# Kernel optimization log

Measured on AMD Instinct MI355X. Metric: run time of the kernel, lower is better.

The kernel has to match this reference:

```python
import jax, jax.numpy as jnp
import numpy as np

H, D, K, V, M = 32, 4096, 128, 128, 8191


def setup_inputs() -> dict:
    key = jax.random.key(0)
    ks = jax.random.split(key, 7)
    return {
        "x": jax.random.normal(ks[0], (D,), jnp.float32),
        "prev_K": jax.random.normal(ks[1], (H, M, K), jnp.float32),
        "prev_V": jax.random.normal(ks[2], (H, M, V), jnp.float32),
        "Wq": jax.random.normal(ks[3], (H, D, K), jnp.float32),
        "Wk": jax.random.normal(ks[4], (H, D, K), jnp.float32),
        "Wv": jax.random.normal(ks[5], (H, D, V), jnp.float32),
        "Wo": jax.random.normal(ks[6], (H, V, D), jnp.float32),
    }


def reference(x, prev_K, prev_V, Wq, Wk, Wv, Wo):
    # Single-token QKV projection
    q = jnp.einsum('d,hdk->hk', x, Wq)              # [h,k]
    k_new = jnp.einsum('d,hdk->hk', x, Wk)[:, None]  # [h,1,k]
    v_new = jnp.einsum('d,hdv->hv', x, Wv)[:, None]  # [h,1,v]
    # KV-cache append
    Kc = jnp.concatenate([prev_K, k_new], axis=1)    # [h,m+1,k]
    Vc = jnp.concatenate([prev_V, v_new], axis=1)    # [h,m+1,v]
    # Attention (no 1/sqrt(k) scaling, matching the original)
    logits = jnp.einsum('hk,hmk->hm', q, Kc)         # [h,m+1]
    weights = jax.nn.softmax(logits, axis=-1)
    o = jnp.einsum('hm,hmv->hv', weights, Vc)        # [h,v]
    # Output projection
    y = jnp.einsum('hv,hvd->d', o, Wo)               # [d]
    return (y, Kc, Vc)
```

## Files before the change

kernel.cpp:

```cpp
#include <hip/hip_runtime.h>
#include <hip/hip_bf16.h>
#include <math.h>

#define H_  32
#define D_  4096
#define K_  128
#define V_  128
#define M_  8191
#define MC_ 8192

typedef float f32x4 __attribute__((ext_vector_type(4)));

__device__ inline f32x4 ntload4(const float* p) {
    return __builtin_nontemporal_load((const f32x4*)p);
}
__device__ inline void ntstore4(float* p, f32x4 v) {
    __builtin_nontemporal_store(v, (f32x4*)p);
}

__device__ inline void atomicMaxF(float* addr, float v) {
    if (v >= 0.f) atomicMax((int*)addr, __float_as_int(v));
    else          atomicMin((unsigned int*)addr, __float_as_uint(v));
}

__global__ void proj_kernel(const float* __restrict__ x,
                            const float* __restrict__ Wq,
                            const float* __restrict__ Wk,
                            const float* __restrict__ Wv,
                            float* __restrict__ qkv ,
                            float* __restrict__ mx  ) {
    const int chunk = blockIdx.x;
    const int h     = blockIdx.y;
    const int proj  = blockIdx.z;
    const float* W  = (proj == 0) ? Wq : ((proj == 1) ? Wk : Wv);
    float* dst      = qkv + proj * (H_ * K_) + h * K_;

    const int t   = threadIdx.x;
    const int grp = t >> 5;
    const int cl  = t & 31;

    if (chunk == 0 && proj == 0 && t == 0) mx[h] = -INFINITY;

    __shared__ float xs[128];
    if (t < 128) xs[t] = x[chunk * 128 + t];
    __syncthreads();

    const float* Wh = W + (size_t)h * D_ * K_ + (size_t)chunk * 128 * K_;

    f32x4 acc = {0.f, 0.f, 0.f, 0.f};
    #pragma unroll 4
    for (int r = grp; r < 128; r += 8) {
        const f32x4 v4 = ntload4(&Wh[(size_t)r * K_ + cl * 4]);
        acc += xs[r] * v4;
    }

    __shared__ float lds[8][K_];
    *(f32x4*)&lds[grp][cl * 4] = acc;
    __syncthreads();
    if (t < K_) {
        float s = 0.f;
        #pragma unroll
        for (int j = 0; j < 8; ++j) s += lds[j][t];
        atomicAdd(&dst[t], s);
    }
}

__global__ void copyK_logits_kernel(const float* __restrict__ prev_K,
                                    const float* __restrict__ qkv,
                                    float* __restrict__ Kc,
                                    float* __restrict__ lg,
                                    float* __restrict__ mx ,
                                    float* __restrict__ o  ,
                                    float* __restrict__ S  ) {
    const int chunk = blockIdx.x;
    const int h     = blockIdx.y;
    const int t     = threadIdx.x;
    const int grp   = t >> 5;
    const int cl    = t & 31;

    if (chunk == 0) {
        if (t < V_) o[h * V_ + t] = 0.f;
        if (t == 0) S[h] = 0.f;
    }

    const float* q  = qkv + h * K_;
    const float* kn = qkv + H_ * K_ + h * K_;
    const f32x4 q4  = *(const f32x4*)&q[cl * 4];

    const float* Ksrc = prev_K + (size_t)h * M_ * K_;
    float*       Kd   = Kc     + (size_t)h * MC_ * K_;
    float*       L    = lg     + (size_t)h * MC_;

    __shared__ float pbuf[64][33];

    #pragma unroll
    for (int r = 0; r < 8; ++r) {
        const int ml = r * 8 + grp;
        const int m  = chunk * 64 + ml;
        const f32x4 v4 = (m == M_) ? *(const f32x4*)&kn[cl * 4]
                                   : ntload4(&Ksrc[(size_t)m * K_ + cl * 4]);
        ntstore4(&Kd[(size_t)m * K_ + cl * 4], v4);
        const f32x4 p4 = v4 * q4;
        pbuf[ml][cl] = p4.x + p4.y + p4.z + p4.w;
    }
    __syncthreads();

    __shared__ float rmax[64];
    if (t < 64) {
        float s = 0.f;
        #pragma unroll
        for (int j = 0; j < 32; ++j) s += pbuf[t][j];
        L[chunk * 64 + t] = s;
        rmax[t] = s;
    }
    __syncthreads();
    if (t == 0) {
        float mm = rmax[0];
        #pragma unroll
        for (int j = 1; j < 64; ++j) mm = fmaxf(mm, rmax[j]);
        atomicMaxF(&mx[h], mm);
    }
}

__global__ void copyV_out_kernel(const float* __restrict__ prev_V,
                                 const float* __restrict__ qkv,
                                 const float* __restrict__ lg,
                                 const float* __restrict__ mx,
                                 float* __restrict__ Vc,
                                 float* __restrict__ o ,
                                 float* __restrict__ S ,
                                 float* __restrict__ y ) {
    const int chunk = blockIdx.x;
    const int h     = blockIdx.y;
    const int t     = threadIdx.x;
    const int grp   = t >> 5;
    const int cl    = t & 31;

    if (chunk == 0 && t < 128) y[h * 128 + t] = 0.f;

    const float MX = mx[h];
    const float* vn   = qkv + 2 * H_ * K_ + h * K_;
    const float* Vsrc = prev_V + (size_t)h * M_ * V_;
    float*       Vd   = Vc     + (size_t)h * MC_ * V_;
    const float* L    = lg     + (size_t)h * MC_;

    f32x4 acc = {0.f, 0.f, 0.f, 0.f};
    #pragma unroll
    for (int r = 0; r < 8; ++r) {
        const int m = chunk * 64 + r * 8 + grp;
        const f32x4 v4 = (m == M_) ? *(const f32x4*)&vn[cl * 4]
                                   : ntload4(&Vsrc[(size_t)m * V_ + cl * 4]);
        ntstore4(&Vd[(size_t)m * V_ + cl * 4], v4);
        const float e = __expf(L[m] - MX);
        acc += e * v4;
    }

    __shared__ float lds[8][V_];
    *(f32x4*)&lds[grp][cl * 4] = acc;

    __shared__ float rsum[64];
    if (t < 64) rsum[t] = __expf(L[chunk * 64 + t] - MX);
    __syncthreads();

    if (t < V_) {
        float s = 0.f;
        #pragma unroll
        for (int j = 0; j < 8; ++j) s += lds[j][t];
        atomicAdd(&o[h * V_ + t], s);
    }
    if (t == 0) {
        float s = 0.f;
        #pragma unroll
        for (int j = 0; j < 64; ++j) s += rsum[j];
        atomicAdd(&S[h], s);
    }
}

__global__ void yproj_kernel(const float* __restrict__ Wo,
                             const float* __restrict__ o,
                             const float* __restrict__ S,
                             float* __restrict__ y) {
    const int chunk = blockIdx.x;
    const int h     = blockIdx.y;
    const int vhalf = blockIdx.z;
    const int t     = threadIdx.x;
    const int wv    = t >> 6;
    const int ln    = t & 63;

    __shared__ float s_inv;
    __shared__ float os[V_ / 2];
    if (t == 0) s_inv = 1.f / S[h];
    __syncthreads();
    if (t < 64) os[t] = o[h * V_ + vhalf * 64 + t] * s_inv;
    __syncthreads();

    const int d0 = chunk * 256 + ln * 4;
    const float* Wh = Wo + (size_t)h * V_ * D_ + (size_t)vhalf * 64 * D_;

    f32x4 acc = {0.f, 0.f, 0.f, 0.f};
    const int v0 = wv * 16;
    #pragma unroll
    for (int v = 0; v < 16; ++v)
        acc += os[v0 + v] * ntload4(&Wh[(size_t)(v0 + v) * D_ + d0]);

    __shared__ f32x4 red4[4][64];
    red4[wv][ln] = acc;
    __syncthreads();
    if (t < 64) {
        const f32x4 s = red4[0][t] + red4[1][t] + red4[2][t] + red4[3][t];
        const int d = chunk * 256 + t * 4;
        atomicAdd(&y[d + 0], s.x);
        atomicAdd(&y[d + 1], s.y);
        atomicAdd(&y[d + 2], s.z);
        atomicAdd(&y[d + 3], s.w);
    }
}

extern "C" void kernel_launch(void* const* d_in, const int* in_sizes, int n_in,
                              void* d_out, int out_size, void* d_ws, size_t ws_size,
                              hipStream_t stream) {
    const float* x      = (const float*)d_in[0];
    const float* prev_K = (const float*)d_in[1];
    const float* prev_V = (const float*)d_in[2];
    const float* Wq     = (const float*)d_in[3];
    const float* Wk     = (const float*)d_in[4];
    const float* Wv     = (const float*)d_in[5];
    const float* Wo     = (const float*)d_in[6];

    float* out = (float*)d_out;
    float* y   = out;
    float* Kc  = out + D_;
    float* Vc  = Kc + (size_t)H_ * MC_ * K_;

    float* ws  = (float*)d_ws;
    float* qkv = ws;
    float* ov  = qkv + 3 * H_ * K_;
    float* Sd  = ov + H_ * V_;
    float* mxd = Sd + H_;
    float* lg  = mxd + H_;

    hipMemsetAsync(qkv, 0, (size_t)3 * H_ * K_ * sizeof(float), stream);

    proj_kernel        <<<dim3(32, H_, 3), 256, 0, stream>>>(x, Wq, Wk, Wv, qkv, mxd);
    copyK_logits_kernel<<<dim3(128, H_),   256, 0, stream>>>(prev_K, qkv, Kc, lg, mxd, ov, Sd);
    copyV_out_kernel   <<<dim3(128, H_),   256, 0, stream>>>(prev_V, qkv, lg, mxd, Vc, ov, Sd, y);
    yproj_kernel       <<<dim3(16, H_, 2), 256, 0, stream>>>(Wo, ov, Sd, y);
}
```

Before: 166.4 us.

## Fuse K-copy/logits and V-copy/output into one flash-decoding split-softmax kernel

```diff
diff --git a/kernel.cpp b/kernel.cpp
--- a/kernel.cpp
+++ b/kernel.cpp
@@ -8,6 +8,7 @@
 #define V_  128
 #define M_  8191
 #define MC_ 8192
+#define NCHUNK_ 64
 
 typedef float f32x4 __attribute__((ext_vector_type(4)));
 
@@ -16,19 +17,13 @@
 }
 __device__ inline void ntstore4(float* p, f32x4 v) {
     __builtin_nontemporal_store(v, (f32x4*)p);
-}
-
-__device__ inline void atomicMaxF(float* addr, float v) {
-    if (v >= 0.f) atomicMax((int*)addr, __float_as_int(v));
-    else          atomicMin((unsigned int*)addr, __float_as_uint(v));
 }
 
 __global__ void proj_kernel(const float* __restrict__ x,
                             const float* __restrict__ Wq,
                             const float* __restrict__ Wk,
                             const float* __restrict__ Wv,
-                            float* __restrict__ qkv ,
-                            float* __restrict__ mx  ) {
+                            float* __restrict__ qkv ) {
     const int chunk = blockIdx.x;
     const int h     = blockIdx.y;
     const int proj  = blockIdx.z;
@@ -39,8 +34,6 @@
     const int grp = t >> 5;
     const int cl  = t & 31;
 
-    if (chunk == 0 && proj == 0 && t == 0) mx[h] = -INFINITY;
-
     __shared__ float xs[128];
     if (t < 128) xs[t] = x[chunk * 128 + t];
     __syncthreads();
@@ -65,114 +58,139 @@
     }
 }
 
-__global__ void copyK_logits_kernel(const float* __restrict__ prev_K,
-                                    const float* __restrict__ qkv,
-                                    float* __restrict__ Kc,
-                                    float* __restrict__ lg,
-                                    float* __restrict__ mx ,
-                                    float* __restrict__ o  ,
-                                    float* __restrict__ S  ) {
+__global__ __launch_bounds__(256) void attn_fused_kernel(
+        const float* __restrict__ prev_K,
+        const float* __restrict__ prev_V,
+        const float* __restrict__ qkv,
+        float* __restrict__ Kc,
+        float* __restrict__ Vc,
+        float* __restrict__ obuf ,
+        float* __restrict__ mxb  ,
+        float* __restrict__ sb   ) {
     const int chunk = blockIdx.x;
     const int h     = blockIdx.y;
     const int t     = threadIdx.x;
     const int grp   = t >> 5;
     const int cl    = t & 31;
 
-    if (chunk == 0) {
-        if (t < V_) o[h * V_ + t] = 0.f;
-        if (t == 0) S[h] = 0.f;
-    }
-
     const float* q  = qkv + h * K_;
     const float* kn = qkv + H_ * K_ + h * K_;
+    const float* vn = qkv + 2 * H_ * K_ + h * K_;
     const f32x4 q4  = *(const f32x4*)&q[cl * 4];
 
     const float* Ksrc = prev_K + (size_t)h * M_ * K_;
     float*       Kd   = Kc     + (size_t)h * MC_ * K_;
-    float*       L    = lg     + (size_t)h * MC_;
-
-    __shared__ float pbuf[64][33];
+
+    __shared__ float pbuf[128][33];
 
     #pragma unroll
-    for (int r = 0; r < 8; ++r) {
+    for (int r = 0; r < 16; ++r) {
         const int ml = r * 8 + grp;
-        const int m  = chunk * 64 + ml;
-        const f32x4 v4 = (m == M_) ? *(const f32x4*)&kn[cl * 4]
-                                   : ntload4(&Ksrc[(size_t)m * K_ + cl * 4]);
+        const int m  = chunk * 128 + ml;
+        f32x4 v4;
+        if (m != M_) v4 = ntload4(&Ksrc[(size_t)m * K_ + cl * 4]);
+        else         v4 = *(const f32x4*)&kn[cl * 4];
         ntstore4(&Kd[(size_t)m * K_ + cl * 4], v4);
         const f32x4 p4 = v4 * q4;
         pbuf[ml][cl] = p4.x + p4.y + p4.z + p4.w;
     }
     __syncthreads();
 
-    __shared__ float rmax[64];
-    if (t < 64) {
+    __shared__ float lrow[128];
+    __shared__ float red[128];
+    if (t < 128) {
         float s = 0.f;
         #pragma unroll
         for (int j = 0; j < 32; ++j) s += pbuf[t][j];
-        L[chunk * 64 + t] = s;
-        rmax[t] = s;
-    }
-    __syncthreads();
+        lrow[t] = s;
+        red[t]  = s;
+    }
+    __syncthreads();
+    for (int s = 64; s > 0; s >>= 1) {
+        if (t < s) red[t] = fmaxf(red[t], red[t + s]);
+        __syncthreads();
+    }
+    const float lmax = red[0];
+    __syncthreads();
+
+    __shared__ float ebuf[128];
+    if (t < 128) {
+        const float e = __expf(lrow[t] - lmax);
+        ebuf[t] = e;
+        red[t]  = e;
+    }
+    __syncthreads();
+    for (int s = 64; s > 0; s >>= 1) {
+        if (t < s) red[t] += red[t + s];
+        __syncthreads();
+    }
     if (t == 0) {
-        float mm = rmax[0];
-        #pragma unroll
-        for (int j = 1; j < 64; ++j) mm = fmaxf(mm, rmax[j]);
-        atomicMaxF(&mx[h], mm);
-    }
-}
-
-__global__ void copyV_out_kernel(const float* __restrict__ prev_V,
-                                 const float* __restrict__ qkv,
-                                 const float* __restrict__ lg,
-                                 const float* __restrict__ mx,
-                                 float* __restrict__ Vc,
-                                 float* __restrict__ o ,
-                                 float* __restrict__ S ,
-                                 float* __restrict__ y ) {
-    const int chunk = blockIdx.x;
-    const int h     = blockIdx.y;
-    const int t     = threadIdx.x;
-    const int grp   = t >> 5;
-    const int cl    = t & 31;
-
-    if (chunk == 0 && t < 128) y[h * 128 + t] = 0.f;
-
-    const float MX = mx[h];
-    const float* vn   = qkv + 2 * H_ * K_ + h * K_;
+        mxb[h * NCHUNK_ + chunk] = lmax;
+        sb [h * NCHUNK_ + chunk] = red[0];
+    }
+
     const float* Vsrc = prev_V + (size_t)h * M_ * V_;
     float*       Vd   = Vc     + (size_t)h * MC_ * V_;
-    const float* L    = lg     + (size_t)h * MC_;
 
     f32x4 acc = {0.f, 0.f, 0.f, 0.f};
     #pragma unroll
-    for (int r = 0; r < 8; ++r) {
-        const int m = chunk * 64 + r * 8 + grp;
-        const f32x4 v4 = (m == M_) ? *(const f32x4*)&vn[cl * 4]
-                                   : ntload4(&Vsrc[(size_t)m * V_ + cl * 4]);
+    for (int r = 0; r < 16; ++r) {
+        const int ml = r * 8 + grp;
+        const int m  = chunk * 128 + ml;
+        f32x4 v4;
+        if (m != M_) v4 = ntload4(&Vsrc[(size_t)m * V_ + cl * 4]);
+        else         v4 = *(const f32x4*)&vn[cl * 4];
         ntstore4(&Vd[(size_t)m * V_ + cl * 4], v4);
-        const float e = __expf(L[m] - MX);
-        acc += e * v4;
-    }
-
-    __shared__ float lds[8][V_];
-    *(f32x4*)&lds[grp][cl * 4] = acc;
-
-    __shared__ float rsum[64];
-    if (t < 64) rsum[t] = __expf(L[chunk * 64 + t] - MX);
-    __syncthreads();
-
+        acc += ebuf[ml] * v4;
+    }
+    __syncthreads();
+    float (*vred)[V_] = (float (*)[V_])pbuf;
+    *(f32x4*)&vred[grp][cl * 4] = acc;
+    __syncthreads();
     if (t < V_) {
         float s = 0.f;
         #pragma unroll
-        for (int j = 0; j < 8; ++j) s += lds[j][t];
-        atomicAdd(&o[h * V_ + t], s);
-    }
+        for (int j = 0; j < 8; ++j) s += vred[j][t];
+        obuf[((size_t)h * NCHUNK_ + chunk) * V_ + t] = s;
+    }
+}
+
+__global__ void combine_kernel(const float* __restrict__ obuf,
+                               const float* __restrict__ mxb,
+                               const float* __restrict__ sb,
+                               float* __restrict__ o ,
+                               float* __restrict__ S ,
+                               float* __restrict__ y ) {
+    const int h = blockIdx.x;
+    const int t = threadIdx.x;
+
+    y[h * 128 + t] = 0.f;
+
+    __shared__ float smx[NCHUNK_];
+    __shared__ float sexp[NCHUNK_];
+    __shared__ float red[NCHUNK_];
+    if (t < NCHUNK_) { smx[t] = mxb[h * NCHUNK_ + t]; red[t] = smx[t]; }
+    __syncthreads();
+    for (int s = NCHUNK_ / 2; s > 0; s >>= 1) {
+        if (t < s) red[t] = fmaxf(red[t], red[t + s]);
+        __syncthreads();
+    }
+    const float MX = red[0];
+    __syncthreads();
+    if (t < NCHUNK_) sexp[t] = __expf(smx[t] - MX);
+    __syncthreads();
+
+    const float* ob = obuf + (size_t)h * NCHUNK_ * V_;
+    float acc = 0.f;
+    #pragma unroll 8
+    for (int c = 0; c < NCHUNK_; ++c) acc += sexp[c] * ob[c * V_ + t];
+    o[h * V_ + t] = acc;
+
     if (t == 0) {
         float s = 0.f;
         #pragma unroll
-        for (int j = 0; j < 64; ++j) s += rsum[j];
-        atomicAdd(&S[h], s);
+        for (int c = 0; c < NCHUNK_; ++c) s += sexp[c] * sb[h * NCHUNK_ + c];
+        S[h] = s;
     }
 }
 
@@ -232,17 +250,19 @@
     float* Kc  = out + D_;
     float* Vc  = Kc + (size_t)H_ * MC_ * K_;
 
-    float* ws  = (float*)d_ws;
-    float* qkv = ws;
-    float* ov  = qkv + 3 * H_ * K_;
-    float* Sd  = ov + H_ * V_;
-    float* mxd = Sd + H_;
-    float* lg  = mxd + H_;
+    float* ws   = (float*)d_ws;
+    float* qkv  = ws;
+    float* obuf = qkv + 3 * H_ * K_;
+    float* mxb  = obuf + (size_t)H_ * NCHUNK_ * V_;
+    float* sb   = mxb + H_ * NCHUNK_;
+    float* ov   = sb + H_ * NCHUNK_;
+    float* Sd   = ov + H_ * V_;
 
     hipMemsetAsync(qkv, 0, (size_t)3 * H_ * K_ * sizeof(float), stream);
 
-    proj_kernel        <<<dim3(32, H_, 3), 256, 0, stream>>>(x, Wq, Wk, Wv, qkv, mxd);
-    copyK_logits_kernel<<<dim3(128, H_),   256, 0, stream>>>(prev_K, qkv, Kc, lg, mxd, ov, Sd);
-    copyV_out_kernel   <<<dim3(128, H_),   256, 0, stream>>>(prev_V, qkv, lg, mxd, Vc, ov, Sd, y);
-    yproj_kernel       <<<dim3(16, H_, 2), 256, 0, stream>>>(Wo, ov, Sd, y);
-}
+    proj_kernel      <<<dim3(32, H_, 3),    256, 0, stream>>>(x, Wq, Wk, Wv, qkv);
+    attn_fused_kernel<<<dim3(NCHUNK_, H_),  256, 0, stream>>>(prev_K, prev_V, qkv,
+                                                              Kc, Vc, obuf, mxb, sb);
+    combine_kernel   <<<H_,                 128, 0, stream>>>(obuf, mxb, sb, ov, Sd, y);
+    yproj_kernel     <<<dim3(16, H_, 2),    256, 0, stream>>>(Wo, ov, Sd, y);
+}
```

Measured after the change: 148.1 us. 1.12x faster.
